# Kernel tuning notes

Measured on AMD Instinct MI355X. Metric: run time of the kernel, lower is better.

## Reference

```python
import jax, jax.numpy as jnp
import numpy as np

B, U, F = 8192, 256, 128

def setup_inputs() -> dict:
    key = jax.random.key(0)
    k1, k2, k3, k4, k5 = jax.random.split(key, 5)
    x = jax.random.normal(k1, (B, F), dtype=jnp.float32)
    # shift ~ RandomNormal(0,1), flat shape [units*F] as in build()
    shift = jax.random.normal(k2, (U * F,), dtype=jnp.float32)
    # semi_axis ~ RandomUniform(0.1, 0.5), constrained >= 1e-5
    semi_axis = 0.1 + 0.4 * jax.random.uniform(k3, (U, F), dtype=jnp.float32)
    # sharpness ~ RandomUniform(0.5, 1.0)
    sharpness = 0.5 + 0.5 * jax.random.uniform(k4, (U,), dtype=jnp.float32)
    # multiplier in {-1, +1} (MinusOrPlusOnesInitializer, p=0.5)
    multiplier = jnp.where(jax.random.uniform(k5, (U,)) > 0.5, 1.0, -1.0).astype(jnp.float32)
    return {"x": x, "shift": shift, "semi_axis": semi_axis,
            "sharpness": sharpness, "multiplier": multiplier}

def reference(x, shift, semi_axis, sharpness, multiplier):
    # out[b,u] = multiplier[u] * sigmoid(sharpness[u] * (1 - sum_f (x[b,f]+shift[u,f])^2 / semi_axis[u,f]^2))
    u, f = semi_axis.shape
    s = shift.reshape(u, f)                       # shift[u*F+f] lines up with reshape in call()
    inv = 1.0 / jnp.square(semi_axis)             # (U,F)
    # Expand (x+s)^2 * inv summed over f as matmuls to avoid the (B,U,F) intermediate.
    quad = (jnp.einsum('bf,uf->bu', jnp.square(x), inv)
            + 2.0 * jnp.einsum('bf,uf->bu', x, s * inv)
            + jnp.sum(jnp.square(s) * inv, axis=1))  # (B,U)
    ellipsoidal = 1.0 - quad
    out = jax.nn.sigmoid(ellipsoidal * sharpness) * multiplier
    return out
```

## Files before the change

### kernel.cpp

```cpp
#include <hip/hip_runtime.h>
#include <math.h>

#define B_N 8192
#define U_N 256
#define F_N 128
#define UG  32
#define BT  128

typedef __attribute__((ext_vector_type(8))) short short8;
typedef __attribute__((ext_vector_type(4))) float f32x4;

static __device__ __forceinline__ unsigned short f2bf(float v) {
  union { float f; unsigned int u; } c; c.f = v;
  unsigned int r = c.u + 0x7fffu + ((c.u >> 16) & 1u);
  return (unsigned short)(r >> 16);
}

__global__ __launch_bounds__(512, 4) void bp_kernel(
    const float* __restrict__ x, const float* __restrict__ shift,
    const float* __restrict__ semi, const float* __restrict__ sharp,
    const float* __restrict__ mult, float* __restrict__ out) {
  __shared__ __align__(16) unsigned short Wf[2][8][64][8];
  __shared__ float Cs[UG];

  const int tid   = threadIdx.x;
  const int lane  = tid & 63;
  const int w     = tid >> 6;
  const int lg    = lane >> 4;
  const int ln    = lane & 15;
  const int btile = blockIdx.x;
  const int u0    = blockIdx.y * UG;

  const int brow0 = btile * BT + w * 16;
  const float* xrow = x + (size_t)(brow0 + ln) * F_N;
  float4 xv[8];
#pragma unroll
  for (int s4 = 0; s4 < 4; ++s4) {
    xv[s4 * 2]     = *reinterpret_cast<const float4*>(xrow + s4 * 32 + lg * 8);
    xv[s4 * 2 + 1] = *reinterpret_cast<const float4*>(xrow + s4 * 32 + lg * 8 + 4);
  }

  {
    const int u_loc = tid >> 4;
    const int f0    = (tid & 15) * 8;
    const float* sp = shift + (size_t)(u0 + u_loc) * F_N + f0;
    const float* ap = semi  + (size_t)(u0 + u_loc) * F_N + f0;
    float4 s0 = *reinterpret_cast<const float4*>(sp);
    float4 s1 = *reinterpret_cast<const float4*>(sp + 4);
    float4 a0 = *reinterpret_cast<const float4*>(ap);
    float4 a1 = *reinterpret_cast<const float4*>(ap + 4);
    float ss[8] = {s0.x, s0.y, s0.z, s0.w, s1.x, s1.y, s1.z, s1.w};
    float aa[8] = {a0.x, a0.y, a0.z, a0.w, a1.x, a1.y, a1.z, a1.w};
    unsigned short qi[8], qb[8];
    float csum = 0.f;
#pragma unroll
    for (int j = 0; j < 8; ++j) {
      float inv = 1.0f / (aa[j] * aa[j]);
      qi[j] = f2bf(inv);
      qb[j] = f2bf(2.0f * ss[j] * inv);
      csum += ss[j] * ss[j] * inv;
    }
    const int tile = u_loc >> 4;
    const int kkp  = f0 >> 5;
    const int lnp  = ((f0 >> 3) & 3) * 16 + (u_loc & 15);
    *reinterpret_cast<uint2*>(&Wf[tile][kkp][lnp][0])     = *reinterpret_cast<uint2*>(qi);
    *reinterpret_cast<uint2*>(&Wf[tile][kkp][lnp][4])     = *reinterpret_cast<uint2*>(qi + 4);
    *reinterpret_cast<uint2*>(&Wf[tile][kkp + 4][lnp][0]) = *reinterpret_cast<uint2*>(qb);
    *reinterpret_cast<uint2*>(&Wf[tile][kkp + 4][lnp][4]) = *reinterpret_cast<uint2*>(qb + 4);
    csum += __shfl_xor(csum, 1, 64);
    csum += __shfl_xor(csum, 2, 64);
    csum += __shfl_xor(csum, 4, 64);
    csum += __shfl_xor(csum, 8, 64);
    if ((lane & 15) == 0) Cs[u_loc] = csum;
  }

  short8 fx2[4], fx1[4];
#pragma unroll
  for (int s4 = 0; s4 < 4; ++s4) {
    float xs[8] = {xv[s4*2].x, xv[s4*2].y, xv[s4*2].z, xv[s4*2].w,
                   xv[s4*2+1].x, xv[s4*2+1].y, xv[s4*2+1].z, xv[s4*2+1].w};
    short8 a2, a1;
#pragma unroll
    for (int j = 0; j < 8; ++j) {
      a2[j] = (short)f2bf(xs[j] * xs[j]);
      a1[j] = (short)f2bf(xs[j]);
    }
    fx2[s4] = a2; fx1[s4] = a1;
  }

  __syncthreads();

  f32x4 acc0 = {0.f, 0.f, 0.f, 0.f};
  f32x4 acc1 = {0.f, 0.f, 0.f, 0.f};
#pragma unroll
  for (int kk = 0; kk < 8; ++kk) {
    short8 a = (kk < 4) ? fx2[kk] : fx1[kk - 4];
    short8 b0 = *reinterpret_cast<const short8*>(&Wf[0][kk][lane][0]);
    short8 b1 = *reinterpret_cast<const short8*>(&Wf[1][kk][lane][0]);
    acc0 = __builtin_amdgcn_mfma_f32_16x16x32_bf16(a, b0, acc0, 0, 0, 0);
    acc1 = __builtin_amdgcn_mfma_f32_16x16x32_bf16(a, b1, acc1, 0, 0, 0);
  }

#pragma unroll
  for (int s = 0; s < 2; ++s) {
    f32x4 acc = s ? acc1 : acc0;
    const int u = u0 + s * 16 + ln;
    const float c  = Cs[s * 16 + ln];
    const float sh = sharp[u];
    const float mu = mult[u];
#pragma unroll
    for (int r = 0; r < 4; ++r) {
      const int b = brow0 + lg * 4 + r;
      float quad = acc[r] + c;
      float z = sh * (1.0f - quad);
      float e = __expf(-z);
      out[(size_t)b * U_N + u] = mu / (1.0f + e);
    }
  }
}

extern "C" void kernel_launch(void* const* d_in, const int* in_sizes, int n_in,
                              void* d_out, int out_size, void* d_ws, size_t ws_size,
                              hipStream_t stream) {
  (void)in_sizes; (void)n_in; (void)out_size; (void)d_ws; (void)ws_size;
  const float* x     = (const float*)d_in[0];
  const float* shift = (const float*)d_in[1];
  const float* semi  = (const float*)d_in[2];
  const float* sharp = (const float*)d_in[3];
  const float* mult  = (const float*)d_in[4];
  float* out = (float*)d_out;

  bp_kernel<<<dim3(B_N / BT, U_N / UG), 512, 0, stream>>>(x, shift, semi, sharp, mult, out);
}
```

Baseline: 13.02 us.

## Retile to 64x64 blocks, swap MFMA operands for vectorized float4 output stores

Changes block tiling from 128 batch rows by 32 units with 512 threads to 64 rows by 64 units with 256 threads, so each wave computes four 16x16 unit tiles. Swapping the MFMA operand order transposes the accumulator, so each lane holds four consecutive units and can write them with one float4 store and read sharpness, multiplier and constants as float4 loads. It also uses the library bf16 conversion and a hardware reciprocal. In exchange, each block now rebuilds twice as many weights, the grid has the same number of blocks but fewer threads each, and the approximate reciprocal may change accuracy slightly.

```diff
diff --git a/kernel.cpp b/kernel.cpp
--- a/kernel.cpp
+++ b/kernel.cpp
@@ -1,37 +1,36 @@
 #include <hip/hip_runtime.h>
+#include <hip/hip_bf16.h>
 #include <math.h>
 
 #define B_N 8192
 #define U_N 256
 #define F_N 128
-#define UG  32
-#define BT  128
+#define UG  64
+#define BT  64
 
 typedef __attribute__((ext_vector_type(8))) short short8;
 typedef __attribute__((ext_vector_type(4))) float f32x4;
 
 static __device__ __forceinline__ unsigned short f2bf(float v) {
-  union { float f; unsigned int u; } c; c.f = v;
-  unsigned int r = c.u + 0x7fffu + ((c.u >> 16) & 1u);
-  return (unsigned short)(r >> 16);
+  __hip_bfloat16 h = __float2bfloat16(v);
+  return *reinterpret_cast<unsigned short*>(&h);
 }
 
-__global__ __launch_bounds__(512, 4) void bp_kernel(
+__global__ __launch_bounds__(256, 4) void bp_kernel(
     const float* __restrict__ x, const float* __restrict__ shift,
     const float* __restrict__ semi, const float* __restrict__ sharp,
     const float* __restrict__ mult, float* __restrict__ out) {
-  __shared__ __align__(16) unsigned short Wf[2][8][64][8];
-  __shared__ float Cs[UG];
+  __shared__ __align__(16) unsigned short Wf[4][8][64][8];
+  __shared__ __align__(16) float Cs[UG];
 
-  const int tid   = threadIdx.x;
-  const int lane  = tid & 63;
-  const int w     = tid >> 6;
-  const int lg    = lane >> 4;
-  const int ln    = lane & 15;
-  const int btile = blockIdx.x;
-  const int u0    = blockIdx.y * UG;
+  const int tid  = threadIdx.x;
+  const int lane = tid & 63;
+  const int w    = tid >> 6;
+  const int lg   = lane >> 4;
+  const int ln   = lane & 15;
+  const int u0   = blockIdx.y * UG;
 
-  const int brow0 = btile * BT + w * 16;
+  const int brow0 = blockIdx.x * BT + w * 16;
   const float* xrow = x + (size_t)(brow0 + ln) * F_N;
   float4 xv[8];
 #pragma unroll
@@ -40,8 +39,9 @@
     xv[s4 * 2 + 1] = *reinterpret_cast<const float4*>(xrow + s4 * 32 + lg * 8 + 4);
   }
 
-  {
-    const int u_loc = tid >> 4;
+#pragma unroll
+  for (int p = 0; p < 4; ++p) {
+    const int u_loc = (tid >> 4) + p * 16;
     const int f0    = (tid & 15) * 8;
     const float* sp = shift + (size_t)(u0 + u_loc) * F_N + f0;
     const float* ap = semi  + (size_t)(u0 + u_loc) * F_N + f0;
@@ -90,32 +90,39 @@
 
   __syncthreads();
 
-  f32x4 acc0 = {0.f, 0.f, 0.f, 0.f};
-  f32x4 acc1 = {0.f, 0.f, 0.f, 0.f};
+  f32x4 acc[4];
+#pragma unroll
+  for (int t = 0; t < 4; ++t) acc[t] = (f32x4){0.f, 0.f, 0.f, 0.f};
 #pragma unroll
   for (int kk = 0; kk < 8; ++kk) {
     short8 a = (kk < 4) ? fx2[kk] : fx1[kk - 4];
-    short8 b0 = *reinterpret_cast<const short8*>(&Wf[0][kk][lane][0]);
-    short8 b1 = *reinterpret_cast<const short8*>(&Wf[1][kk][lane][0]);
-    acc0 = __builtin_amdgcn_mfma_f32_16x16x32_bf16(a, b0, acc0, 0, 0, 0);
-    acc1 = __builtin_amdgcn_mfma_f32_16x16x32_bf16(a, b1, acc1, 0, 0, 0);
+#pragma unroll
+    for (int t = 0; t < 4; ++t) {
+      short8 wv = *reinterpret_cast<const short8*>(&Wf[t][kk][lane][0]);
+      acc[t] = __builtin_amdgcn_mfma_f32_16x16x32_bf16(wv, a, acc[t], 0, 0, 0);
+    }
   }
 
+  const int brow = brow0 + ln;
 #pragma unroll
-  for (int s = 0; s < 2; ++s) {
-    f32x4 acc = s ? acc1 : acc0;
-    const int u = u0 + s * 16 + ln;
-    const float c  = Cs[s * 16 + ln];
-    const float sh = sharp[u];
-    const float mu = mult[u];
+  for (int t = 0; t < 4; ++t) {
+    const int ub = t * 16 + lg * 4;
+    const float4 c  = *reinterpret_cast<const float4*>(&Cs[ub]);
+    const float4 sh = *reinterpret_cast<const float4*>(&sharp[u0 + ub]);
+    const float4 mu = *reinterpret_cast<const float4*>(&mult[u0 + ub]);
+    const float cc[4] = {c.x, c.y, c.z, c.w};
+    const float shs[4] = {sh.x, sh.y, sh.z, sh.w};
+    const float mus[4] = {mu.x, mu.y, mu.z, mu.w};
+    float res[4];
 #pragma unroll
     for (int r = 0; r < 4; ++r) {
-      const int b = brow0 + lg * 4 + r;
-      float quad = acc[r] + c;
-      float z = sh * (1.0f - quad);
+      float quad = acc[t][r] + cc[r];
+      float z = shs[r] * (1.0f - quad);
       float e = __expf(-z);
-      out[(size_t)b * U_N + u] = mu / (1.0f + e);
+      res[r] = mus[r] * __builtin_amdgcn_rcpf(1.0f + e);
     }
+    *reinterpret_cast<float4*>(&out[(size_t)brow * U_N + u0 + ub]) =
+        make_float4(res[0], res[1], res[2], res[3]);
   }
 }
 
@@ -130,5 +137,5 @@
   const float* mult  = (const float*)d_in[4];
   float* out = (float*)d_out;
 
-  bp_kernel<<<dim3(B_N / BT, U_N / UG), 512, 0, stream>>>(x, shift, semi, sharp, mult, out);
+  bp_kernel<<<dim3(B_N / BT, U_N / UG), 256, 0, stream>>>(x, shift, semi, sharp, mult, out);
 }
```

Result: slower. 13.86 us (+6.5%).
